# Kernel optimization log

Hardware: AMD Instinct MI355X
Metric: run time of the kernel (lower is better)

The kernel has to match this reference:

```python
import jax, jax.numpy as jnp
import numpy as np

BEAMS = (1, 3, 1, 5, 1)
DIM_CAT, DIM_SOL, DIM_RG, H, M = 54, 87, 235, 1024, 256
BATCH = 8192


def setup_inputs():
    key = jax.random.key(0)
    keys = iter(jax.random.split(key, 96))
    s = 0.02

    def lin(din, dout):
        return (jax.random.normal(next(keys), (din, dout), jnp.float32) * s,
                jax.random.normal(next(keys), (dout,), jnp.float32) * s)

    inp = {"features": jax.random.normal(next(keys), (BATCH, H), jnp.float32)}
    inp["Wc"], inp["bc"] = lin(DIM_CAT, M)
    inp["Ws1"], inp["bs1"] = lin(DIM_SOL, M)
    inp["Ws2"], inp["bs2"] = lin(DIM_SOL, M)
    inp["Wr"], inp["br"] = lin(DIM_RG, M)
    outs = (DIM_CAT, DIM_SOL, DIM_SOL, DIM_RG, DIM_RG)
    for i in range(5):
        inp["Wh1_%d" % i], inp["bh1_%d" % i] = lin(H + i * M, H)
        inp["Wh2_%d" % i], inp["bh2_%d" % i] = lin(H, H)
        inp["Wo_%d" % i], inp["bo_%d" % i] = lin(H, outs[i])
    return inp


def _beam_search(features, in_params, hid_params):
    # Vectorized equivalent of the python beam loops: all combinatorial beam
    # indices of a stage are folded into one batched MLP pass.
    b0, b1, b2, b3, b4 = BEAMS
    B = features.shape[0]

    def msg(oh, j):  # one-hot [B,n,D] -> message [B,n,M]  (self.inputs[j])
        W, b = in_params[j]
        return jax.nn.relu(oh @ W + b)

    def stage(i, msgs, n, k):
        feat = jnp.broadcast_to(features[:, None, :], (B, n, H))
        x = jnp.concatenate([feat] + msgs, axis=-1)
        Wh1, bh1, Wh2, bh2, Wo, bo = hid_params[i]
        h = jax.nn.relu(x @ Wh1 + bh1)
        h = jnp.tanh(h @ Wh2 + bh2)
        p = jax.nn.softmax(h @ Wo + bo, axis=-1)
        sc, ix = jax.lax.top_k(p, k)  # [B,n,k]
        return sc.reshape(B, n * k), ix.reshape(B, n * k)

    s0, i0 = stage(0, [], 1, b0)
    oh0 = jax.nn.one_hot(i0, DIM_CAT, dtype=features.dtype)

    s1, i1 = stage(1, [msg(oh0, 0)], b0, b1)
    oh1 = jax.nn.one_hot(i1, DIM_SOL, dtype=features.dtype)

    n2 = b0 * b1
    ix = jnp.arange(n2)
    s2, i2 = stage(2, [msg(oh0[:, ix // b1], 0), msg(oh1[:, ix], 1)], n2, b2)
    oh2 = jax.nn.one_hot(i2, DIM_SOL, dtype=features.dtype)

    n3 = n2 * b2
    ix = jnp.arange(n3)
    s3, i3 = stage(3, [msg(oh0[:, ix // (b1 * b2)], 0),
                       msg(oh1[:, ix // b2], 1),
                       msg(oh2[:, ix], 2)], n3, b3)
    oh3 = jax.nn.one_hot(i3, DIM_RG, dtype=features.dtype)

    n4 = n3 * b3
    ix = jnp.arange(n4)
    s4, i4 = stage(4, [msg(oh0[:, ix // (b1 * b2 * b3)], 0),
                       msg(oh1[:, ix // (b2 * b3)], 1),
                       msg(oh2[:, ix // b3], 2),
                       msg(oh3[:, ix], 3)], n4, b4)

    # expansion factors (== torch .repeat(...).reshape pattern)
    f = (b1 * b2 * b3 * b4, b2 * b3 * b4, b3 * b4, b4)
    rep = lambda a, r: jnp.repeat(a, r, axis=1)
    topk = jnp.stack([rep(i0, f[0]), rep(i1, f[1]), rep(i2, f[2]),
                      rep(i3, f[3]), i4], axis=-1)  # [B,K,5]
    score = rep(s0, f[0]) * rep(s1, f[1]) * rep(s2, f[2]) * rep(s3, f[3]) * s4
    order = jnp.argsort(-score, axis=-1)  # descending sort of joint scores
    score_sorted = jnp.take_along_axis(score, order, axis=-1)
    topk = jnp.take_along_axis(topk, order[..., None], axis=1)
    return topk, score_sorted


def reference(features, Wc, bc, Ws1, bs1, Ws2, bs2, Wr, br,
              Wh1_0, bh1_0, Wh2_0, bh2_0, Wo_0, bo_0,
              Wh1_1, bh1_1, Wh2_1, bh2_1, Wo_1, bo_1,
              Wh1_2, bh1_2, Wh2_2, bh2_2, Wo_2, bo_2,
              Wh1_3, bh1_3, Wh2_3, bh2_3, Wo_3, bo_3,
              Wh1_4, bh1_4, Wh2_4, bh2_4, Wo_4, bo_4):
    in_params = [(Wc, bc), (Ws1, bs1), (Ws2, bs2), (Wr, br)]
    hid_params = [
        (Wh1_0, bh1_0, Wh2_0, bh2_0, Wo_0, bo_0),
        (Wh1_1, bh1_1, Wh2_1, bh2_1, Wo_1, bo_1),
        (Wh1_2, bh1_2, Wh2_2, bh2_2, Wo_2, bo_2),
        (Wh1_3, bh1_3, Wh2_3, bh2_3, Wo_3, bo_3),
        (Wh1_4, bh1_4, Wh2_4, bh2_4, Wo_4, bo_4),
    ]
    topk, _ = _beam_search(features, in_params, hid_params)
    return topk
```

## Files before the change

kernel.cpp:

```cpp
#include <hip/hip_runtime.h>
#include <math.h>

#define NB 8192
enum { ACT_NONE = 0, ACT_RELU = 1, ACT_TANH = 2 };

typedef double d4_t __attribute__((ext_vector_type(4)));

template<typename TA, int ACT, bool HB, bool HA>
__global__ __launch_bounds__(256)
void mgemm_k(const TA* __restrict__ A, int lda,
             const float* __restrict__ W,
             const float* __restrict__ bias,
             const double* __restrict__ addsrc,
             double* __restrict__ C, int K)
{
    __shared__ double Al[16][129];
    __shared__ double Bl[16][128];
    const int tid  = threadIdx.x;
    const int lane = tid & 63;
    const int w    = tid >> 6;
    const int q    = lane >> 4;
    const int c    = lane & 15;
    const int m0w  = (w >> 1) * 64;
    const int n0w  = (w & 1) * 64;
    const size_t m0 = (size_t)blockIdx.y * 128;
    const int    n0 = blockIdx.x * 128;

    const int srow  = tid >> 1;
    const int shalf = tid & 1;
    const int bk    = tid >> 4;
    const int bseg  = tid & 15;

    d4_t acc[4][4];
#pragma unroll
    for (int i = 0; i < 4; i++)
#pragma unroll
        for (int j = 0; j < 4; j++) acc[i][j] = (d4_t){0.0, 0.0, 0.0, 0.0};

    for (int kt = 0; kt < K; kt += 16) {
        {
            const TA* ap = A + (m0 + srow) * (size_t)lda + kt + shalf * 8;
#pragma unroll
            for (int e = 0; e < 8; e++)
                Al[shalf * 8 + e][srow] = (double)ap[e];
        }
        {
            const float* wp = W + (size_t)(kt + bk) * 1024 + n0 + bseg;
#pragma unroll
            for (int e = 0; e < 8; e++)
                Bl[bk][bseg + 16 * e] = (double)wp[16 * e];
        }
        __syncthreads();
#pragma unroll
        for (int kk = 0; kk < 4; kk++) {
            double a[4], b[4];
#pragma unroll
            for (int i = 0; i < 4; i++) a[i] = Al[kk * 4 + q][m0w + i * 16 + c];
#pragma unroll
            for (int j = 0; j < 4; j++) b[j] = Bl[kk * 4 + q][n0w + j * 16 + c];
#pragma unroll
            for (int i = 0; i < 4; i++)
#pragma unroll
                for (int j = 0; j < 4; j++)
                    acc[i][j] = __builtin_amdgcn_mfma_f64_16x16x4f64(
                        a[i], b[j], acc[i][j], 0, 0, 0);
        }
        __syncthreads();
    }

#pragma unroll
    for (int i = 0; i < 4; i++)
#pragma unroll
        for (int j = 0; j < 4; j++)
#pragma unroll
            for (int v = 0; v < 4; v++) {
                size_t gr = m0 + m0w + i * 16 + q * 4 + v;
                int    gc = n0 + n0w + j * 16 + c;
                double val = acc[i][j][v];
                if (HB) val += (double)bias[gc];
                if (HA) val += addsrc[gr * 1024 + gc];
                if (ACT == ACT_RELU) val = val > 0.0 ? val : 0.0;
                if (ACT == ACT_TANH) val = tanh(val);
                C[gr * 1024 + gc] = val;
            }
}

__global__ void msg_build_d(const float* __restrict__ Wt, const float* __restrict__ bias,
                            const int* __restrict__ idx, int istride, int ioff,
                            double* __restrict__ out, int ldo, int ooff)
{
    int b = blockIdx.x;
    int j = threadIdx.x;
    int id = idx[(size_t)b * istride + ioff];
    double v = (double)Wt[(size_t)id * 256 + j] + (double)bias[j];
    out[(size_t)b * ldo + ooff + j] = v > 0.0 ? v : 0.0;
}

__global__ __launch_bounds__(256)
void wo_topk(const double* __restrict__ h2,
             const float* __restrict__ W,
             const float* __restrict__ bo,
             int N, int k,
             float* __restrict__ sout, int sstride, int soff,
             int* __restrict__ iout, int istride, int ioff)
{
    __shared__ double h2s[8][1024];
    __shared__ double dred[256];
    __shared__ float  pred[256];
    __shared__ int    ired[256];
    const int tid = threadIdx.x;
    const size_t rbase = (size_t)blockIdx.x * 8;

    for (int t = tid; t < 8192; t += 256)
        h2s[t >> 10][t & 1023] = h2[(rbase + (t >> 10)) * 1024 + (t & 1023)];
    __syncthreads();

    const int c = tid;
    double a[8] = {0, 0, 0, 0, 0, 0, 0, 0};
    if (c < N) {
        for (int kk = 0; kk < 1024; kk++) {
            double wv = (double)W[(size_t)kk * N + c];
#pragma unroll
            for (int r = 0; r < 8; r++)
                a[r] = fma(h2s[r][kk], wv, a[r]);
        }
    }
    double bb = (c < N) ? (double)bo[c] : 0.0;

    for (int r = 0; r < 8; r++) {
        double lgv = a[r] + bb;
        dred[tid] = (c < N) ? lgv : -INFINITY;
        __syncthreads();
        for (int s = 128; s; s >>= 1) {
            if (tid < s) dred[tid] = fmax(dred[tid], dred[tid + s]);
            __syncthreads();
        }
        double mx = dred[0];
        __syncthreads();
        double e = (c < N) ? exp(lgv - mx) : 0.0;
        dred[tid] = e;
        __syncthreads();
        for (int s = 128; s; s >>= 1) {
            if (tid < s) dred[tid] += dred[tid + s];
            __syncthreads();
        }
        double se = dred[0];
        __syncthreads();
        float p = (c < N) ? (float)(e / se) : -1.f;

        for (int kk = 0; kk < k; kk++) {
            pred[tid] = p;
            ired[tid] = (c < N) ? c : (1 << 20);
            __syncthreads();
            for (int s = 128; s; s >>= 1) {
                if (tid < s) {
                    float ov = pred[tid + s]; int oi = ired[tid + s];
                    if (ov > pred[tid] || (ov == pred[tid] && oi < ired[tid])) {
                        pred[tid] = ov; ired[tid] = oi;
                    }
                }
                __syncthreads();
            }
            if (tid == 0) {
                size_t b = rbase + r;
                sout[b * sstride + soff + kk] = pred[0];
                iout[b * istride + ioff + kk] = ired[0];
            }
            int win = ired[0];
            __syncthreads();
            if (c == win) p = -1.f;
        }
    }
}

__global__ void finalize_q(const float* __restrict__ s0, const float* __restrict__ s1,
                           const float* __restrict__ s2, const float* __restrict__ s3,
                           const float* __restrict__ s4,
                           const int* __restrict__ i0, const int* __restrict__ i1,
                           const int* __restrict__ i2, const int* __restrict__ i3,
                           const int* __restrict__ i4,
                           int* __restrict__ out)
{
    int b = blockIdx.x * 256 + threadIdx.x;
    float sc[15];
    float a0 = s0[b];
    for (int t = 0; t < 15; t++) {
        int a = t / 5;
        float v = a0 * s1[b * 3 + a];
        v = v * s2[b * 3 + a];
        v = v * s3[b * 15 + t];
        v = v * s4[b * 15 + t];
        sc[t] = v;
    }
    bool used[15] = {false};
    for (int r = 0; r < 15; r++) {
        int best = -1; float bv = -INFINITY;
        for (int t = 0; t < 15; t++)
            if (!used[t] && sc[t] > bv) { bv = sc[t]; best = t; }
        used[best] = true;
        int a = best / 5;
        int* o = out + (size_t)b * 75 + r * 5;
        o[0] = i0[b];
        o[1] = i1[b * 3 + a];
        o[2] = i2[b * 3 + a];
        o[3] = i3[b * 15 + best];
        o[4] = i4[b * 15 + best];
    }
}

static void dgemm(hipStream_t st, int a_is_f32, const void* A, int lda,
                  const float* W, const float* bias,
                  const double* add, double* C,
                  int rows, int K, int act)
{
    dim3 grid(8, rows / 128);
#define LK(TA, AC, HBv, HAv) hipLaunchKernelGGL((mgemm_k<TA, AC, HBv, HAv>), grid, dim3(256), 0, st, \
        (const TA*)A, lda, W, bias, add, C, K)
#define ACTS(TA, HBv, HAv) do { if (act == 0) LK(TA, 0, HBv, HAv); \
                                else if (act == 1) LK(TA, 1, HBv, HAv); \
                                else LK(TA, 2, HBv, HAv); } while (0)
#define BDISP(TA) do { if (bias) { if (add) ACTS(TA, true, true); else ACTS(TA, true, false); } \
                       else      { if (add) ACTS(TA, false, true); else ACTS(TA, false, false); } } while (0)
    if (a_is_f32) BDISP(float); else BDISP(double);
#undef BDISP
#undef ACTS
#undef LK
}

extern "C" void kernel_launch(void* const* d_in, const int* in_sizes, int n_in,
                              void* d_out, int out_size, void* d_ws, size_t ws_size,
                              hipStream_t stream)
{
    (void)in_sizes; (void)n_in; (void)out_size;
    const float* feat = (const float*)d_in[0];
    const float* Wc  = (const float*)d_in[1];
    const float* bc  = (const float*)d_in[2];
    const float* Ws1 = (const float*)d_in[3];
    const float* bs1 = (const float*)d_in[4];
    const float* Ws2 = (const float*)d_in[5];
    const float* bs2 = (const float*)d_in[6];
    const float* Wr  = (const float*)d_in[7];
    const float* br  = (const float*)d_in[8];
    auto Wh1 = [&](int i) { return (const float*)d_in[9 + 6 * i]; };
    auto bh1 = [&](int i) { return (const float*)d_in[10 + 6 * i]; };
    auto Wh2 = [&](int i) { return (const float*)d_in[11 + 6 * i]; };
    auto bh2 = [&](int i) { return (const float*)d_in[12 + 6 * i]; };
    auto Wo  = [&](int i) { return (const float*)d_in[13 + 6 * i]; };
    auto bo  = [&](int i) { return (const float*)d_in[14 + 6 * i]; };
    const int outs[5] = {54, 87, 87, 235, 235};

    const size_t perRow = 6144ull * 8 + 37ull * 4 + 37ull * 4;
    int R = NB;
    while (R > 256 && (size_t)R * perRow > ws_size) R >>= 1;

    double* ws = (double*)d_ws;
    size_t off = 0;
    auto alloc = [&](size_t n) { double* p = ws + off; off += n; return p; };
    double* msg0 = alloc((size_t)R * 256);
    double* xm0  = alloc((size_t)R * 512);
    double* xm1  = alloc((size_t)R * 512);
    double* xm2  = alloc((size_t)R * 512);
    double* xms[3] = {xm0, xm1, xm2};
    double* bufC = alloc((size_t)R * 1024);
    double* base = alloc((size_t)R * 1024);
    double* h1   = alloc((size_t)R * 1024);
    double* h2   = alloc((size_t)R * 1024);
    double* m3   = alloc((size_t)R * 256);
    float* fbase = (float*)(ws + off);
    float* s0 = fbase;            float* s1 = fbase + R;
    float* s2 = s1 + 3 * R;       float* s3 = s2 + 3 * R;
    float* s4 = s3 + 15 * R;
    int* ibase = (int*)(s4 + 15 * R);
    int* i0 = ibase;              int* i1 = ibase + R;
    int* i2 = i1 + 3 * R;         int* i3 = i2 + 3 * R;
    int* i4 = i3 + 15 * R;

    dim3 wg(R / 8);

    for (int r0 = 0; r0 < NB; r0 += R) {
        const float* fC = feat + (size_t)r0 * 1024;

        dgemm(stream, 1, fC, 1024, Wh1(0), bh1(0), nullptr, h1, R, 1024, ACT_RELU);
        dgemm(stream, 0, h1, 1024, Wh2(0), bh2(0), nullptr, h2, R, 1024, ACT_TANH);
        hipLaunchKernelGGL(wo_topk, wg, dim3(256), 0, stream, h2, Wo(0), bo(0), outs[0], 1, s0, 1, 0, i0, 1, 0);
        hipLaunchKernelGGL(msg_build_d, dim3(R), dim3(256), 0, stream, Wc, bc, i0, 1, 0, msg0, 256, 0);

        dgemm(stream, 1, fC, 1024, Wh1(1), nullptr, nullptr, bufC, R, 1024, ACT_NONE);
        dgemm(stream, 0, msg0, 256, Wh1(1) + (size_t)1024 * 1024, bh1(1), bufC, h1, R, 256, ACT_RELU);
        dgemm(stream, 0, h1, 1024, Wh2(1), bh2(1), nullptr, h2, R, 1024, ACT_TANH);
        hipLaunchKernelGGL(wo_topk, wg, dim3(256), 0, stream, h2, Wo(1), bo(1), outs[1], 3, s1, 3, 0, i1, 3, 0);
        for (int a = 0; a < 3; a++)
            hipLaunchKernelGGL(msg_build_d, dim3(R), dim3(256), 0, stream, Ws1, bs1, i1, 3, a, xms[a], 512, 0);

        dgemm(stream, 1, fC, 1024, Wh1(2), nullptr, nullptr, bufC, R, 1024, ACT_NONE);
        dgemm(stream, 0, msg0, 256, Wh1(2) + (size_t)1024 * 1024, nullptr, bufC, bufC, R, 256, ACT_NONE);
        for (int a = 0; a < 3; a++) {
            dgemm(stream, 0, xms[a], 512, Wh1(2) + (size_t)1280 * 1024, bh1(2), bufC, h1, R, 256, ACT_RELU);
            dgemm(stream, 0, h1, 1024, Wh2(2), bh2(2), nullptr, h2, R, 1024, ACT_TANH);
            hipLaunchKernelGGL(wo_topk, wg, dim3(256), 0, stream, h2, Wo(2), bo(2), outs[2], 1, s2, 3, a, i2, 3, a);
        }
        for (int a = 0; a < 3; a++)
            hipLaunchKernelGGL(msg_build_d, dim3(R), dim3(256), 0, stream, Ws2, bs2, i2, 3, a, xms[a], 512, 256);

        dgemm(stream, 1, fC, 1024, Wh1(3), nullptr, nullptr, bufC, R, 1024, ACT_NONE);
        dgemm(stream, 0, msg0, 256, Wh1(3) + (size_t)1024 * 1024, nullptr, bufC, bufC, R, 256, ACT_NONE);
        for (int a = 0; a < 3; a++) {
            dgemm(stream, 0, xms[a], 512, Wh1(3) + (size_t)1280 * 1024, bh1(3), bufC, h1, R, 512, ACT_RELU);
            dgemm(stream, 0, h1, 1024, Wh2(3), bh2(3), nullptr, h2, R, 1024, ACT_TANH);
            hipLaunchKernelGGL(wo_topk, wg, dim3(256), 0, stream, h2, Wo(3), bo(3), outs[3], 5, s3, 15, 5 * a, i3, 15, 5 * a);
        }

        dgemm(stream, 1, fC, 1024, Wh1(4), nullptr, nullptr, bufC, R, 1024, ACT_NONE);
        dgemm(stream, 0, msg0, 256, Wh1(4) + (size_t)1024 * 1024, nullptr, bufC, bufC, R, 256, ACT_NONE);
        for (int a = 0; a < 3; a++) {
            dgemm(stream, 0, xms[a], 512, Wh1(4) + (size_t)1280 * 1024, nullptr, bufC, base, R, 512, ACT_NONE);
            for (int c = 0; c < 5; c++) {
                int t = a * 5 + c;
                hipLaunchKernelGGL(msg_build_d, dim3(R), dim3(256), 0, stream, Wr, br, i3, 15, t, m3, 256, 0);
                dgemm(stream, 0, m3, 256, Wh1(4) + (size_t)1792 * 1024, bh1(4), base, h1, R, 256, ACT_RELU);
                dgemm(stream, 0, h1, 1024, Wh2(4), bh2(4), nullptr, h2, R, 1024, ACT_TANH);
                hipLaunchKernelGGL(wo_topk, wg, dim3(256), 0, stream, h2, Wo(4), bo(4), outs[4], 1, s4, 15, t, i4, 15, t);
            }
        }

        hipLaunchKernelGGL(finalize_q, dim3(R / 256), dim3(256), 0, stream,
                           s0, s1, s2, s3, s4, i0, i1, i2, i3, i4, (int*)d_out + (size_t)r0 * 75);
    }
}
```

Before: 21.97 ms.

## Fuse message gather into GEMM A-loads and batch beam branches per stage

Removes the separate msg_build kernels: the GEMM now builds one-hot message rows on the fly by gathering rows of the embedding table indexed by the beam indices, adding bias and applying relu while loading the A tile. Beam branches (3 or 5 per stage) are stacked along the row dimension with a z index derived from the row, so each stage runs one large GEMM and one top-k launch instead of a loop of small launches. The K tile is doubled to 32 to halve the number of barriers per tile. The trade-off is larger workspace buffers (5x h1/h2), which may force a smaller row chunk, and a branch inside the A-load path.

Result: slower. 27.79 ms (+26.5%).

```diff
diff --git a/kernel.cpp b/kernel.cpp
--- a/kernel.cpp
+++ b/kernel.cpp
@@ -6,16 +6,26 @@
 
 typedef double d4_t __attribute__((ext_vector_type(4)));
 
+struct GSet {
+    const float* T;
+    const float* bT;
+    const int*   idx;
+    int is, io, iz;
+};
+
 template<typename TA, int ACT, bool HB, bool HA>
 __global__ __launch_bounds__(256)
-void mgemm_k(const TA* __restrict__ A, int lda,
-             const float* __restrict__ W,
-             const float* __restrict__ bias,
-             const double* __restrict__ addsrc,
-             double* __restrict__ C, int K)
-{
-    __shared__ double Al[16][129];
-    __shared__ double Bl[16][128];
+void mgemm2(const TA* __restrict__ A, int lda, int KA,
+            const float* __restrict__ W,
+            const float* __restrict__ bias,
+            const double* __restrict__ addsrc, unsigned amask,
+            double* __restrict__ C, int K,
+            unsigned rmask, int rlog,
+            GSet g0, GSet g1)
+{
+    __shared__ double Al[32][129];
+    __shared__ double Bl[32][128];
+    __shared__ int idc[2][128];
     const int tid  = threadIdx.x;
     const int lane = tid & 63;
     const int w    = tid >> 6;
@@ -25,11 +35,18 @@
     const int n0w  = (w & 1) * 64;
     const size_t m0 = (size_t)blockIdx.y * 128;
     const int    n0 = blockIdx.x * 128;
-
-    const int srow  = tid >> 1;
-    const int shalf = tid & 1;
-    const int bk    = tid >> 4;
-    const int bseg  = tid & 15;
+    const int z = (int)(m0 >> rlog);
+
+    const int srow = tid >> 1;
+    const int half = tid & 1;
+    const int bk   = tid >> 3;
+    const int bc   = tid & 7;
+
+    const int ns = (K - KA) >> 8;
+    if (ns > 0 && tid < 128)
+        idc[0][tid] = g0.idx[(size_t)((m0 + tid) & rmask) * g0.is + g0.io + z * g0.iz];
+    if (ns > 1 && tid >= 128 && tid < 256)
+        idc[1][tid - 128] = g1.idx[(size_t)((m0 + tid - 128) & rmask) * g1.is + g1.io + z * g1.iz];
 
     d4_t acc[4][4];
 #pragma unroll
@@ -37,22 +54,39 @@
 #pragma unroll
         for (int j = 0; j < 4; j++) acc[i][j] = (d4_t){0.0, 0.0, 0.0, 0.0};
 
-    for (int kt = 0; kt < K; kt += 16) {
+    __syncthreads();
+
+    for (int kt = 0; kt < K; kt += 32) {
         {
-            const TA* ap = A + (m0 + srow) * (size_t)lda + kt + shalf * 8;
-#pragma unroll
-            for (int e = 0; e < 8; e++)
-                Al[shalf * 8 + e][srow] = (double)ap[e];
+            const int kb = kt + half * 16;
+            if (kb + 16 <= KA) {
+                const TA* ap = A + (m0 + srow) * (size_t)lda + kb;
+#pragma unroll
+                for (int e = 0; e < 16; e++)
+                    Al[half * 16 + e][srow] = (double)ap[e];
+            } else {
+                const int koff = kb - KA;
+                const int s = koff >> 8;
+                const int lk = koff & 255;
+                const GSet& g = s ? g1 : g0;
+                const float* tp = g.T + (size_t)idc[s][srow] * 256 + lk;
+                const float* bp = g.bT + lk;
+#pragma unroll
+                for (int e = 0; e < 16; e++) {
+                    double v = (double)tp[e] + (double)bp[e];
+                    Al[half * 16 + e][srow] = v > 0.0 ? v : 0.0;
+                }
+            }
         }
         {
-            const float* wp = W + (size_t)(kt + bk) * 1024 + n0 + bseg;
-#pragma unroll
-            for (int e = 0; e < 8; e++)
-                Bl[bk][bseg + 16 * e] = (double)wp[16 * e];
-        }
-        __syncthreads();
-#pragma unroll
-        for (int kk = 0; kk < 4; kk++) {
+            const float* wp = W + (size_t)(kt + bk) * 1024 + n0 + bc;
+#pragma unroll
+            for (int e = 0; e < 16; e++)
+                Bl[bk][bc + 8 * e] = (double)wp[8 * e];
+        }
+        __syncthreads();
+#pragma unroll
+        for (int kk = 0; kk < 8; kk++) {
             double a[4], b[4];
 #pragma unroll
             for (int i = 0; i < 4; i++) a[i] = Al[kk * 4 + q][m0w + i * 16 + c];
@@ -78,31 +112,20 @@
                 int    gc = n0 + n0w + j * 16 + c;
                 double val = acc[i][j][v];
                 if (HB) val += (double)bias[gc];
-                if (HA) val += addsrc[gr * 1024 + gc];
+                if (HA) val += addsrc[(size_t)(gr & amask) * 1024 + gc];
                 if (ACT == ACT_RELU) val = val > 0.0 ? val : 0.0;
                 if (ACT == ACT_TANH) val = tanh(val);
                 C[gr * 1024 + gc] = val;
             }
 }
 
-__global__ void msg_build_d(const float* __restrict__ Wt, const float* __restrict__ bias,
-                            const int* __restrict__ idx, int istride, int ioff,
-                            double* __restrict__ out, int ldo, int ooff)
-{
-    int b = blockIdx.x;
-    int j = threadIdx.x;
-    int id = idx[(size_t)b * istride + ioff];
-    double v = (double)Wt[(size_t)id * 256 + j] + (double)bias[j];
-    out[(size_t)b * ldo + ooff + j] = v > 0.0 ? v : 0.0;
-}
-
 __global__ __launch_bounds__(256)
 void wo_topk(const double* __restrict__ h2,
-             const float* __restrict__ W,
-             const float* __restrict__ bo,
+             const float* __restrict__ W, const float* __restrict__ bo,
              int N, int k,
-             float* __restrict__ sout, int sstride, int soff,
-             int* __restrict__ iout, int istride, int ioff)
+             float* __restrict__ sout, int* __restrict__ iout,
+             int stride, int soff, int zmul,
+             unsigned rmask, int rlog)
 {
     __shared__ double h2s[8][1024];
     __shared__ double dred[256];
@@ -128,6 +151,9 @@
     double bb = (c < N) ? (double)bo[c] : 0.0;
 
     for (int r = 0; r < 8; r++) {
+        size_t row = rbase + r;
+        size_t b = row & rmask;
+        int    z = (int)(row >> rlog);
         double lgv = a[r] + bb;
         dred[tid] = (c < N) ? lgv : -INFINITY;
         __syncthreads();
@@ -162,9 +188,9 @@
                 __syncthreads();
             }
             if (tid == 0) {
-                size_t b = rbase + r;
-                sout[b * sstride + soff + kk] = pred[0];
-                iout[b * istride + ioff + kk] = ired[0];
+                int off = soff + z * zmul + kk;
+                sout[b * stride + off] = pred[0];
+                iout[b * stride + off] = ired[0];
             }
             int win = ired[0];
             __syncthreads();
@@ -208,14 +234,17 @@
     }
 }
 
-static void dgemm(hipStream_t st, int a_is_f32, const void* A, int lda,
-                  const float* W, const float* bias,
-                  const double* add, double* C,
-                  int rows, int K, int act)
+static const GSet GNULL = {nullptr, nullptr, nullptr, 0, 0, 0};
+
+static void mm(hipStream_t st, int a_is_f32, const void* A, int lda, int KA,
+               const float* W, const float* bias,
+               const double* add, unsigned amask,
+               double* C, int K, int rows, unsigned rmask, int rlog,
+               GSet g0, GSet g1, int act)
 {
     dim3 grid(8, rows / 128);
-#define LK(TA, AC, HBv, HAv) hipLaunchKernelGGL((mgemm_k<TA, AC, HBv, HAv>), grid, dim3(256), 0, st, \
-        (const TA*)A, lda, W, bias, add, C, K)
+#define LK(TA, AC, HBv, HAv) hipLaunchKernelGGL((mgemm2<TA, AC, HBv, HAv>), grid, dim3(256), 0, st, \
+        (const TA*)A, lda, KA, W, bias, add, amask, C, K, rmask, rlog, g0, g1)
 #define ACTS(TA, HBv, HAv) do { if (act == 0) LK(TA, 0, HBv, HAv); \
                                 else if (act == 1) LK(TA, 1, HBv, HAv); \
                                 else LK(TA, 2, HBv, HAv); } while (0)
@@ -249,23 +278,18 @@
     auto bo  = [&](int i) { return (const float*)d_in[14 + 6 * i]; };
     const int outs[5] = {54, 87, 87, 235, 235};
 
-    const size_t perRow = 6144ull * 8 + 37ull * 4 + 37ull * 4;
-    int R = NB;
-    while (R > 256 && (size_t)R * perRow > ws_size) R >>= 1;
+    const size_t perRow = 11264ull * 8 + 37ull * 4 + 37ull * 4;
+    int R = NB, rlog = 13;
+    while (R > 1024 && (size_t)R * perRow > ws_size) { R >>= 1; rlog--; }
+    const unsigned rmask = (unsigned)(R - 1);
 
     double* ws = (double*)d_ws;
     size_t off = 0;
     auto alloc = [&](size_t n) { double* p = ws + off; off += n; return p; };
-    double* msg0 = alloc((size_t)R * 256);
-    double* xm0  = alloc((size_t)R * 512);
-    double* xm1  = alloc((size_t)R * 512);
-    double* xm2  = alloc((size_t)R * 512);
-    double* xms[3] = {xm0, xm1, xm2};
     double* bufC = alloc((size_t)R * 1024);
-    double* base = alloc((size_t)R * 1024);
-    double* h1   = alloc((size_t)R * 1024);
-    double* h2   = alloc((size_t)R * 1024);
-    double* m3   = alloc((size_t)R * 256);
+    double* h1b  = alloc((size_t)R * 5 * 1024);
+    double* h2b  = alloc((size_t)R * 5 * 1024);
+    double* base = h2b + (size_t)4 * R * 1024;
     float* fbase = (float*)(ws + off);
     float* s0 = fbase;            float* s1 = fbase + R;
     float* s2 = s1 + 3 * R;       float* s3 = s2 + 3 * R;
@@ -275,52 +299,55 @@
     int* i2 = i1 + 3 * R;         int* i3 = i2 + 3 * R;
     int* i4 = i3 + 15 * R;
 
-    dim3 wg(R / 8);
-
     for (int r0 = 0; r0 < NB; r0 += R) {
         const float* fC = feat + (size_t)r0 * 1024;
-
-        dgemm(stream, 1, fC, 1024, Wh1(0), bh1(0), nullptr, h1, R, 1024, ACT_RELU);
-        dgemm(stream, 0, h1, 1024, Wh2(0), bh2(0), nullptr, h2, R, 1024, ACT_TANH);
-        hipLaunchKernelGGL(wo_topk, wg, dim3(256), 0, stream, h2, Wo(0), bo(0), outs[0], 1, s0, 1, 0, i0, 1, 0);
-        hipLaunchKernelGGL(msg_build_d, dim3(R), dim3(256), 0, stream, Wc, bc, i0, 1, 0, msg0, 256, 0);
-
-        dgemm(stream, 1, fC, 1024, Wh1(1), nullptr, nullptr, bufC, R, 1024, ACT_NONE);
-        dgemm(stream, 0, msg0, 256, Wh1(1) + (size_t)1024 * 1024, bh1(1), bufC, h1, R, 256, ACT_RELU);
-        dgemm(stream, 0, h1, 1024, Wh2(1), bh2(1), nullptr, h2, R, 1024, ACT_TANH);
-        hipLaunchKernelGGL(wo_topk, wg, dim3(256), 0, stream, h2, Wo(1), bo(1), outs[1], 3, s1, 3, 0, i1, 3, 0);
-        for (int a = 0; a < 3; a++)
-            hipLaunchKernelGGL(msg_build_d, dim3(R), dim3(256), 0, stream, Ws1, bs1, i1, 3, a, xms[a], 512, 0);
-
-        dgemm(stream, 1, fC, 1024, Wh1(2), nullptr, nullptr, bufC, R, 1024, ACT_NONE);
-        dgemm(stream, 0, msg0, 256, Wh1(2) + (size_t)1024 * 1024, nullptr, bufC, bufC, R, 256, ACT_NONE);
+        auto WOT = [&](const double* h2, int st, int rows, int N, int k,
+                       float* so, int* io_, int stride, int soff, int zmul) {
+            (void)st;
+            hipLaunchKernelGGL(wo_topk, dim3(rows / 8), dim3(256), 0, stream,
+                               h2, Wo(st), bo(st), N, k, so, io_, stride, soff, zmul, rmask, rlog);
+        };
+
+        mm(stream, 1, fC, 1024, 1024, Wh1(0), bh1(0), nullptr, 0, h1b, 1024, R, rmask, rlog, GNULL, GNULL, ACT_RELU);
+        mm(stream, 0, h1b, 1024, 1024, Wh2(0), bh2(0), nullptr, 0, h2b, 1024, R, rmask, rlog, GNULL, GNULL, ACT_TANH);
+        WOT(h2b, 0, R, outs[0], 1, s0, i0, 1, 0, 0);
+
+        GSet gm0 = {Wc, bc, i0, 1, 0, 0};
+
+        mm(stream, 1, fC, 1024, 1024, Wh1(1), bh1(1), nullptr, 0, h1b, 1280, R, rmask, rlog, gm0, GNULL, ACT_RELU);
+        mm(stream, 0, h1b, 1024, 1024, Wh2(1), bh2(1), nullptr, 0, h2b, 1024, R, rmask, rlog, GNULL, GNULL, ACT_TANH);
+        WOT(h2b, 1, R, outs[1], 3, s1, i1, 3, 0, 0);
+
+        mm(stream, 1, fC, 1024, 1024, Wh1(2), nullptr, nullptr, 0, bufC, 1280, R, rmask, rlog, gm0, GNULL, ACT_NONE);
+        {
+            GSet g = {Ws1, bs1, i1, 3, 0, 1};
+            mm(stream, 1, nullptr, 0, 0, Wh1(2) + (size_t)1280 * 1024, bh1(2), bufC, rmask,
+               h1b, 256, 3 * R, rmask, rlog, g, GNULL, ACT_RELU);
+        }
+        mm(stream, 0, h1b, 1024, 1024, Wh2(2), bh2(2), nullptr, 0, h2b, 1024, 3 * R, rmask, rlog, GNULL, GNULL, ACT_TANH);
+        WOT(h2b, 2, 3 * R, outs[2], 1, s2, i2, 3, 0, 1);
+
+        mm(stream, 1, fC, 1024, 1024, Wh1(3), nullptr, nullptr, 0, bufC, 1280, R, rmask, rlog, gm0, GNULL, ACT_NONE);
+        {
+            GSet ga = {Ws1, bs1, i1, 3, 0, 1};
+            GSet gb = {Ws2, bs2, i2, 3, 0, 1};
+            mm(stream, 1, nullptr, 0, 0, Wh1(3) + (size_t)1280 * 1024, bh1(3), bufC, rmask,
+               h1b, 512, 3 * R, rmask, rlog, ga, gb, ACT_RELU);
+        }
+        mm(stream, 0, h1b, 1024, 1024, Wh2(3), bh2(3), nullptr, 0, h2b, 1024, 3 * R, rmask, rlog, GNULL, GNULL, ACT_TANH);
+        WOT(h2b, 3, 3 * R, outs[3], 5, s3, i3, 15, 0, 5);
+
+        mm(stream, 1, fC, 1024, 1024, Wh1(4), nullptr, nullptr, 0, bufC, 1280, R, rmask, rlog, gm0, GNULL, ACT_NONE);
         for (int a = 0; a < 3; a++) {
-            dgemm(stream, 0, xms[a], 512, Wh1(2) + (size_t)1280 * 1024, bh1(2), bufC, h1, R, 256, ACT_RELU);
-            dgemm(stream, 0, h1, 1024, Wh2(2), bh2(2), nullptr, h2, R, 1024, ACT_TANH);
-            hipLaunchKernelGGL(wo_topk, wg, dim3(256), 0, stream, h2, Wo(2), bo(2), outs[2], 1, s2, 3, a, i2, 3, a);
-        }
-        for (int a = 0; a < 3; a++)
-            hipLaunchKernelGGL(msg_build_d, dim3(R), dim3(256), 0, stream, Ws2, bs2, i2, 3, a, xms[a], 512, 256);
-
-        dgemm(stream, 1, fC, 1024, Wh1(3), nullptr, nullptr, bufC, R, 1024, ACT_NONE);
-        dgemm(stream, 0, msg0, 256, Wh1(3) + (size_t)1024 * 1024, nullptr, bufC, bufC, R, 256, ACT_NONE);
-        for (int a = 0; a < 3; a++) {
-            dgemm(stream, 0, xms[a], 512, Wh1(3) + (size_t)1280 * 1024, bh1(3), bufC, h1, R, 512, ACT_RELU);
-            dgemm(stream, 0, h1, 1024, Wh2(3), bh2(3), nullptr, h2, R, 1024, ACT_TANH);
-            hipLaunchKernelGGL(wo_topk, wg, dim3(256), 0, stream, h2, Wo(3), bo(3), outs[3], 5, s3, 15, 5 * a, i3, 15, 5 * a);
-        }
-
-        dgemm(stream, 1, fC, 1024, Wh1(4), nullptr, nullptr, bufC, R, 1024, ACT_NONE);
-        dgemm(stream, 0, msg0, 256, Wh1(4) + (size_t)1024 * 1024, nullptr, bufC, bufC, R, 256, ACT_NONE);
-        for (int a = 0; a < 3; a++) {
-            dgemm(stream, 0, xms[a], 512, Wh1(4) + (size_t)1280 * 1024, nullptr, bufC, base, R, 512, ACT_NONE);
-            for (int c = 0; c < 5; c++) {
-                int t = a * 5 + c;
-                hipLaunchKernelGGL(msg_build_d, dim3(R), dim3(256), 0, stream, Wr, br, i3, 15, t, m3, 256, 0);
-                dgemm(stream, 0, m3, 256, Wh1(4) + (size_t)1792 * 1024, bh1(4), base, h1, R, 256, ACT_RELU);
-                dgemm(stream, 0, h1, 1024, Wh2(4), bh2(4), nullptr, h2, R, 1024, ACT_TANH);
-                hipLaunchKernelGGL(wo_topk, wg, dim3(256), 0, stream, h2, Wo(4), bo(4), outs[4], 1, s4, 15, t, i4, 15, t);
-            }
+            GSet ga = {Ws1, bs1, i1, 3, a, 0};
+            GSet gb = {Ws2, bs2, i2, 3, a, 0};
+            mm(stream, 1, nullptr, 0, 0, Wh1(4) + (size_t)1280 * 1024, nullptr, bufC, rmask,
+               base, 512, R, rmask, rlog, ga, gb, ACT_NONE);
+            GSet gr_ = {Wr, br, i3, 15, 5 * a, 1};
+            mm(stream, 1, nullptr, 0, 0, Wh1(4) + (size_t)1792 * 1024, bh1(4), base, rmask,
+               h1b, 256, 5 * R, rmask, rlog, gr_, GNULL, ACT_RELU);
+            mm(stream, 0, h1b, 1024, 1024, Wh2(4), bh2(4), nullptr, 0, h2b, 1024, 5 * R, rmask, rlog, GNULL, GNULL, ACT_TANH);
+            WOT(h2b, 4, 5 * R, outs[4], 1, s4, i4, 15, 5 * a, 1);
         }
 
         hipLaunchKernelGGL(finalize_q, dim3(R / 256), dim3(256), 0, stream,
```
